# Performance work log

Hardware: AMD Instinct MI355X
Metric: run time of the kernel (lower is better)

## Reference

```python
import jax, jax.numpy as jnp
import numpy as np

LEAK_RATE = 0.1
SPIKE_THRESHOLD = 0.5
MAX_DIM = 2560
R = 2048   # reservoir dim
D = 1024   # input dim
B = 4096   # batch


def setup_inputs() -> dict:
    key = jax.random.key(0)
    k1, k2, k3, k4, k5 = jax.random.split(key, 5)
    inputs = jax.random.normal(k1, (B, D), dtype=jnp.float32)
    prev_state = jax.random.normal(k2, (B, MAX_DIM), dtype=jnp.float32)
    W_in = jax.random.normal(k3, (R, D), dtype=jnp.float32) * (1.0 / np.sqrt(D))
    W_res = jax.random.normal(k4, (R, R), dtype=jnp.float32) * (1.0 / np.sqrt(R))
    W_gate = jax.random.normal(k5, (3 * R, D), dtype=jnp.float32) * (1.0 / np.sqrt(D))
    return {"inputs": inputs, "prev_state": prev_state,
            "W_in": W_in, "W_res": W_res, "W_gate": W_gate}


def reference(inputs, prev_state, W_in, W_res, W_gate):
    # Slice state to active reservoir width (W_res.shape[0] == R)
    prev = prev_state[:, :R]                                  # [B, R]
    input_part = jnp.matmul(inputs, W_in.T)                   # [B, R]
    reservoir_part = jnp.matmul(prev, W_res.T)                # [B, R]
    gate = jax.nn.sigmoid(jnp.matmul(inputs, W_gate.T))       # [B, 3R]
    i_gate, f_gate, o_gate = jnp.split(gate, 3, axis=-1)      # each [B, R]
    state = (1.0 - LEAK_RATE) * (f_gate * prev) \
        + LEAK_RATE * jnp.tanh(i_gate * (input_part + reservoir_part))
    state = o_gate * state
    # Spike threshold + soft reset
    state = jnp.where(state > SPIKE_THRESHOLD, state - SPIKE_THRESHOLD, state)
    # Pad up to max dynamic reservoir dim
    padded = jnp.pad(state, ((0, 0), (0, MAX_DIM - R)))       # [B, MAX_DIM]
    return padded
```

## Files before the change

### kernel.cpp

```cpp
#include <hip/hip_runtime.h>
#include <stdint.h>

#define B_  4096
#define D_  1024
#define R_  2048
#define MAXD 2560

typedef _Float16 half8 __attribute__((ext_vector_type(8)));
typedef _Float16 half4 __attribute__((ext_vector_type(4)));
typedef float    f32x4 __attribute__((ext_vector_type(4)));

constexpr int BM = 128;
constexpr int BN = 64;
constexpr int BK = 32;
constexpr int NCH1 = D_ / BK;
constexpr int NCH2 = R_ / BK;

constexpr size_t XF_OFF  = 0;
constexpr size_t PF_OFF  = XF_OFF  + (size_t)256 * 32 * 2 * 512;
constexpr size_t WIF_OFF = PF_OFF  + (size_t)256 * 64 * 2 * 512;
constexpr size_t WRF_OFF = WIF_OFF + (size_t)128 * 32 * 2 * 512;
constexpr size_t WGF_OFF = WRF_OFF + (size_t)128 * 64 * 2 * 512;
constexpr size_t WS_HALVES = WGF_OFF + (size_t)384 * 32 * 2 * 512;
constexpr size_t WS_BYTES  = WS_HALVES * 2;
constexpr int NPACK_WTASKS = 49152;
constexpr int NPAD_WTASKS  = 8192;

__device__ __forceinline__ float sigmoidf_(float x) { return 1.0f / (1.0f + expf(-x)); }

__device__ __forceinline__ void gload_lds16(const _Float16* g, _Float16* l) {
    typedef const uint32_t __attribute__((address_space(1)))* gp_t;
    typedef uint32_t __attribute__((address_space(3)))* lp_t;
    __builtin_amdgcn_global_load_lds((gp_t)(const void*)g, (lp_t)(void*)l, 16, 0, 0);
}

__global__ __launch_bounds__(256)
void prep(const float* __restrict__ X, const float* __restrict__ P,
          const float* __restrict__ Win, const float* __restrict__ Wres,
          const float* __restrict__ Wg, _Float16* __restrict__ ws,
          float* __restrict__ out)
{
    const int l = threadIdx.x & 63;
    const int wtask = blockIdx.x * 4 + (threadIdx.x >> 6);
    if (wtask < NPACK_WTASKS) {
        const float* src; int ld, rg, kb;
        int cp = wtask;
        if (cp < 8192)       {              src = X;    ld = D_;   rg = cp >> 5; kb = cp & 31; }
        else if (cp < 24576) { cp -= 8192;  src = P;    ld = MAXD; rg = cp >> 6; kb = cp & 63; }
        else if (cp < 28672) { cp -= 24576; src = Win;  ld = D_;   rg = cp >> 5; kb = cp & 31; }
        else if (cp < 36864) { cp -= 28672; src = Wres; ld = R_;   rg = cp >> 6; kb = cp & 63; }
        else                 { cp -= 36864; src = Wg;   ld = D_;   rg = cp >> 5; kb = cp & 31; }
        const float* s = src + (size_t)(rg * 16 + (l & 15)) * ld + kb * 32 + (l >> 4) * 8;
        f32x4 v0 = *(const f32x4*)s;
        f32x4 v1 = *(const f32x4*)(s + 4);
        half8 h, lo;
        #pragma unroll
        for (int j = 0; j < 4; ++j) {
            h[j]     = (_Float16)v0[j];  lo[j]     = (_Float16)(v0[j] - (float)h[j]);
            h[4 + j] = (_Float16)v1[j];  lo[4 + j] = (_Float16)(v1[j] - (float)h[4 + j]);
        }
        _Float16* dst = ws + (size_t)wtask * 1024;
        *(half8*)(dst + l * 8) = h;
        *(half8*)(dst + 512 + l * 8) = lo;
    } else {
        int p2 = wtask - NPACK_WTASKS;
        size_t idx = (size_t)p2 * 256 + l * 4;
        size_t row = idx >> 9, col = idx & 511;
        *(f32x4*)(out + row * MAXD + R_ + col) = (f32x4){0.f, 0.f, 0.f, 0.f};
    }
}

__global__ __launch_bounds__(256, 2)
void reservoir_packed(const _Float16* __restrict__ ws,
                      const float* __restrict__ P,
                      float* __restrict__ out)
{
    __shared__ _Float16 smem[32768];

    const int tid  = threadIdx.x;
    const int lane = tid & 63;
    const int wv   = tid >> 6;
    const int m0   = blockIdx.y * BM;
    const int n0   = blockIdx.x * BN;
    const int lb   = lane * 8;
    const int rgA  = (m0 >> 4) + wv * 2;
    const int ng0  = n0 >> 4;

    f32x4 acc[4][2][4];
    #pragma unroll
    for (int s = 0; s < 4; ++s)
        #pragma unroll
        for (int mt = 0; mt < 2; ++mt)
            #pragma unroll
            for (int nt = 0; nt < 4; ++nt) acc[s][mt][nt] = (f32x4){0.f, 0.f, 0.f, 0.f};

    auto dmaW1 = [&](int t, int buf) {
        #pragma unroll
        for (int i = 0; i < 8; ++i) {
            const int c = wv * 8 + i, pl = c >> 4, r = c & 15, s = r >> 2, g = r & 3;
            const size_t gh = (s == 0)
                ? WIF_OFF + ((size_t)((ng0 + g) * 32 + t) * 2 + pl) * 512
                : WGF_OFF + ((size_t)(((s - 1) * 128 + ng0 + g) * 32 + t) * 2 + pl) * 512;
            gload_lds16(ws + gh + lb, &smem[buf * 16384 + pl * 8192 + r * 512]);
        }
    };
    auto dmaW2 = [&](int t, int buf) {
        #pragma unroll
        for (int i = 0; i < 2; ++i) {
            const int c = wv * 2 + i, pl = c >> 2, g = c & 3;
            const size_t gh = WRF_OFF + ((size_t)((ng0 + g) * 64 + t) * 2 + pl) * 512;
            gload_lds16(ws + gh + lb, &smem[buf * 16384 + pl * 8192 + g * 512]);
        }
    };

#define LDA(ROFF, KBS, T, H0, L0, H1, L1)                                                         \
    {                                                                                             \
        const _Float16* b0_ = ws + (ROFF) + ((size_t)((rgA + 0) * (KBS) + (T)) * 2) * 512 + lb;   \
        const _Float16* b1_ = ws + (ROFF) + ((size_t)((rgA + 1) * (KBS) + (T)) * 2) * 512 + lb;   \
        H0 = *(const half8*)b0_;  L0 = *(const half8*)(b0_ + 512);                                \
        H1 = *(const half8*)b1_;  L1 = *(const half8*)(b1_ + 512);                                \
    }

#define MBLK(BB, NSETS, AH0, AL0, AH1, AL1)                                                       \
    {                                                                                             \
        __builtin_amdgcn_s_setprio(1);                                                            \
        _Pragma("unroll")                                                                         \
        for (int s = 0; s < (NSETS); ++s) {                                                       \
            _Pragma("unroll")                                                                     \
            for (int nt = 0; nt < 4; ++nt) {                                                      \
                half8 bh = *(const half8*)&smem[(BB) + (s * 4 + nt) * 512 + lb];                  \
                half8 bl = *(const half8*)&smem[(BB) + 8192 + (s * 4 + nt) * 512 + lb];           \
                acc[s][0][nt] = __builtin_amdgcn_mfma_f32_16x16x32_f16(AH0, bh, acc[s][0][nt], 0, 0, 0); \
                acc[s][0][nt] = __builtin_amdgcn_mfma_f32_16x16x32_f16(AL0, bh, acc[s][0][nt], 0, 0, 0); \
                acc[s][0][nt] = __builtin_amdgcn_mfma_f32_16x16x32_f16(AH0, bl, acc[s][0][nt], 0, 0, 0); \
                acc[s][1][nt] = __builtin_amdgcn_mfma_f32_16x16x32_f16(AH1, bh, acc[s][1][nt], 0, 0, 0); \
                acc[s][1][nt] = __builtin_amdgcn_mfma_f32_16x16x32_f16(AL1, bh, acc[s][1][nt], 0, 0, 0); \
                acc[s][1][nt] = __builtin_amdgcn_mfma_f32_16x16x32_f16(AH1, bl, acc[s][1][nt], 0, 0, 0); \
            }                                                                                     \
        }                                                                                         \
        __builtin_amdgcn_s_setprio(0);                                                            \
    }

#define BARR()                                                                                    \
    {                                                                                             \
        __builtin_amdgcn_sched_barrier(0);                                                        \
        asm volatile("s_waitcnt vmcnt(4) lgkmcnt(0)" ::: "memory");                               \
        __builtin_amdgcn_s_barrier();                                                             \
        __builtin_amdgcn_sched_barrier(0);                                                        \
    }
#define FENCE() __builtin_amdgcn_sched_barrier(0)

    half8 ah0A, al0A, ah1A, al1A, ah0B, al0B, ah1B, al1B;

    dmaW1(0, 0);
    FENCE();
    LDA(XF_OFF, 32, 0, ah0A, al0A, ah1A, al1A);
    BARR();

    #pragma unroll 1
    for (int t = 0; t < NCH1 - 2; t += 2) {
        dmaW1(t + 1, 1); FENCE(); LDA(XF_OFF, 32, t + 1, ah0B, al0B, ah1B, al1B);
        MBLK(0, 4, ah0A, al0A, ah1A, al1A)
        BARR();
        dmaW1(t + 2, 0); FENCE(); LDA(XF_OFF, 32, t + 2, ah0A, al0A, ah1A, al1A);
        MBLK(16384, 4, ah0B, al0B, ah1B, al1B)
        BARR();
    }
    dmaW1(31, 1); FENCE(); LDA(XF_OFF, 32, 31, ah0B, al0B, ah1B, al1B);
    MBLK(0, 4, ah0A, al0A, ah1A, al1A)
    BARR();
    dmaW2(0, 0); FENCE(); LDA(PF_OFF, 64, 0, ah0A, al0A, ah1A, al1A);
    MBLK(16384, 4, ah0B, al0B, ah1B, al1B)
    BARR();

    #pragma unroll 1
    for (int t = 0; t < NCH2 - 2; t += 2) {
        dmaW2(t + 1, 1); FENCE(); LDA(PF_OFF, 64, t + 1, ah0B, al0B, ah1B, al1B);
        MBLK(0, 1, ah0A, al0A, ah1A, al1A)
        BARR();
        dmaW2(t + 2, 0); FENCE(); LDA(PF_OFF, 64, t + 2, ah0A, al0A, ah1A, al1A);
        MBLK(16384, 1, ah0B, al0B, ah1B, al1B)
        BARR();
    }
    dmaW2(63, 1); FENCE(); LDA(PF_OFF, 64, 63, ah0B, al0B, ah1B, al1B);
    MBLK(0, 1, ah0A, al0A, ah1A, al1A)
    BARR();
    MBLK(16384, 1, ah0B, al0B, ah1B, al1B)

#undef MBLK
#undef LDA
#undef BARR
#undef FENCE

    const int fr = lane & 15;
    const int qd = lane >> 4;
    #pragma unroll
    for (int mt = 0; mt < 2; ++mt)
        #pragma unroll
        for (int nt = 0; nt < 4; ++nt)
            #pragma unroll
            for (int r = 0; r < 4; ++r) {
                int row = m0 + wv * 32 + mt * 16 + qd * 4 + r;
                int col = n0 + nt * 16 + fr;
                float pre = acc[0][mt][nt][r];
                float ig  = sigmoidf_(acc[1][mt][nt][r]);
                float fg  = sigmoidf_(acc[2][mt][nt][r]);
                float og  = sigmoidf_(acc[3][mt][nt][r]);
                float pv  = P[(size_t)row * MAXD + col];
                float st  = 0.9f * (fg * pv) + 0.1f * tanhf(ig * pre);
                st *= og;
                if (st > 0.5f) st -= 0.5f;
                out[(size_t)row * MAXD + col] = st;
            }
}

__device__ __forceinline__ void wg_barrier_ref() {
    __builtin_amdgcn_sched_barrier(0);
    asm volatile("s_waitcnt lgkmcnt(0)" ::: "memory");
    __builtin_amdgcn_s_barrier();
    __builtin_amdgcn_sched_barrier(0);
}

__global__ __launch_bounds__(256, 2)
void reservoir_ref(const float* __restrict__ X, const float* __restrict__ P,
                   const float* __restrict__ Win, const float* __restrict__ Wres,
                   const float* __restrict__ Wg, float* __restrict__ out)
{
    __shared__ _Float16 sA[2][8][512];
    __shared__ _Float16 sW[2][4][4][512];
    const int tid  = threadIdx.x;
    const int lane = tid & 63;
    const int wv   = tid >> 6;
    const int m0   = blockIdx.y * BM;
    const int n0   = blockIdx.x * BN;
    f32x4 acc[4][2][4];
    #pragma unroll
    for (int s = 0; s < 4; ++s)
        #pragma unroll
        for (int mt = 0; mt < 2; ++mt)
            #pragma unroll
            for (int nt = 0; nt < 4; ++nt) acc[s][mt][nt] = (f32x4){0.f, 0.f, 0.f, 0.f};
    const int crow = tid >> 3;
    const int c4   = (tid & 7) * 4;
    const int q    = c4 >> 3;
    const int fbase = q * 128 + (c4 & 4);
    const int raddr = ((((lane & 15) ^ (lane >> 4)) << 3) + ((lane >> 4) << 7));
    f32x4 pa[4];
    f32x4 pw[8];
    auto issue_loads = [&](int t) {
        if (t < NCH1) {
            const int kc = t * BK + c4;
            const float* a = X + (size_t)m0 * D_ + kc;
            #pragma unroll
            for (int i = 0; i < 4; ++i) pa[i] = *(const f32x4*)(a + (size_t)(crow + 32 * i) * D_);
            const float* w = Win + (size_t)n0 * D_ + kc;
            #pragma unroll
            for (int i = 0; i < 2; ++i) pw[i] = *(const f32x4*)(w + (size_t)(crow + 32 * i) * D_);
            const float* g = Wg + (size_t)n0 * D_ + kc;
            #pragma unroll
            for (int gg = 0; gg < 3; ++gg)
                #pragma unroll
                for (int i = 0; i < 2; ++i)
                    pw[2 + gg * 2 + i] = *(const f32x4*)(g + (size_t)(gg * R_ + crow + 32 * i) * D_);
        } else {
            const int kc = t * BK - D_ + c4;
            const float* a = P + (size_t)m0 * MAXD + kc;
            #pragma unroll
            for (int i = 0; i < 4; ++i) pa[i] = *(const f32x4*)(a + (size_t)(crow + 32 * i) * MAXD);
            const float* w = Wres + (size_t)n0 * R_ + kc;
            #pragma unroll
            for (int i = 0; i < 2; ++i) pw[i] = *(const f32x4*)(w + (size_t)(crow + 32 * i) * R_);
        }
    };
    auto stage_A = [&]() {
        #pragma unroll
        for (int i = 0; i < 4; ++i) {
            const int r = crow + 32 * i;
            const int idx = (((r & 15) ^ q) << 3) + fbase;
            half4 h, l;
            #pragma unroll
            for (int j = 0; j < 4; ++j) {
                float v = pa[i][j];
                h[j] = (_Float16)v;
                l[j] = (_Float16)(v - (float)h[j]);
            }
            *(half4*)(&sA[0][r >> 4][idx]) = h;
            *(half4*)(&sA[1][r >> 4][idx]) = l;
        }
    };
    auto stage_W = [&](int nw) {
        #pragma unroll
        for (int i = 0; i < 8; ++i) if (i < nw) {
            const int s   = (i < 2) ? 0 : 1 + ((i - 2) >> 1);
            const int sub = (i < 2) ? i : ((i - 2) & 1);
            const int r   = crow + 32 * sub;
            const int idx = (((r & 15) ^ q) << 3) + fbase;
            half4 h, l;
            #pragma unroll
            for (int j = 0; j < 4; ++j) {
                float v = pw[i][j];
                h[j] = (_Float16)v;
                l[j] = (_Float16)(v - (float)h[j]);
            }
            *(half4*)(&sW[0][s][r >> 4][idx]) = h;
            *(half4*)(&sW[1][s][r >> 4][idx]) = l;
        }
    };
#define RMFMA(NSETS)                                                                              \
    {                                                                                             \
        half8 ah0 = *(const half8*)(&sA[0][wv * 2 + 0][raddr]);                                   \
        half8 al0 = *(const half8*)(&sA[1][wv * 2 + 0][raddr]);                                   \
        half8 ah1 = *(const half8*)(&sA[0][wv * 2 + 1][raddr]);                                   \
        half8 al1 = *(const half8*)(&sA[1][wv * 2 + 1][raddr]);                                   \
        _Pragma("unroll")                                                                         \
        for (int s = 0; s < NSETS; ++s) {                                                         \
            _Pragma("unroll")                                                                     \
            for (int nt = 0; nt < 4; ++nt) {                                                      \
                half8 bh = *(const half8*)(&sW[0][s][nt][raddr]);                                 \
                half8 bl = *(const half8*)(&sW[1][s][nt][raddr]);                                 \
                acc[s][0][nt] = __builtin_amdgcn_mfma_f32_16x16x32_f16(ah0, bh, acc[s][0][nt], 0, 0, 0); \
                acc[s][0][nt] = __builtin_amdgcn_mfma_f32_16x16x32_f16(al0, bh, acc[s][0][nt], 0, 0, 0); \
                acc[s][0][nt] = __builtin_amdgcn_mfma_f32_16x16x32_f16(ah0, bl, acc[s][0][nt], 0, 0, 0); \
                acc[s][1][nt] = __builtin_amdgcn_mfma_f32_16x16x32_f16(ah1, bh, acc[s][1][nt], 0, 0, 0); \
                acc[s][1][nt] = __builtin_amdgcn_mfma_f32_16x16x32_f16(al1, bh, acc[s][1][nt], 0, 0, 0); \
                acc[s][1][nt] = __builtin_amdgcn_mfma_f32_16x16x32_f16(ah1, bl, acc[s][1][nt], 0, 0, 0); \
            }                                                                                     \
        }                                                                                         \
    }
    issue_loads(0);
    #pragma unroll 1
    for (int t = 0; t < NCH1; ++t) {
        stage_A(); stage_W(8);
        issue_loads(t + 1);
        wg_barrier_ref();
        RMFMA(4)
        wg_barrier_ref();
    }
    #pragma unroll 1
    for (int t = NCH1; t < NCH1 + NCH2; ++t) {
        stage_A(); stage_W(2);
        if (t + 1 < NCH1 + NCH2) issue_loads(t + 1);
        wg_barrier_ref();
        RMFMA(1)
        wg_barrier_ref();
    }
#undef RMFMA
    const int fr = lane & 15;
    const int qd = lane >> 4;
    #pragma unroll
    for (int mt = 0; mt < 2; ++mt)
        #pragma unroll
        for (int nt = 0; nt < 4; ++nt)
            #pragma unroll
            for (int r = 0; r < 4; ++r) {
                int row = m0 + wv * 32 + mt * 16 + qd * 4 + r;
                int col = n0 + nt * 16 + fr;
                float pre = acc[0][mt][nt][r];
                float ig  = sigmoidf_(acc[1][mt][nt][r]);
                float fg  = sigmoidf_(acc[2][mt][nt][r]);
                float og  = sigmoidf_(acc[3][mt][nt][r]);
                float pv  = P[(size_t)row * MAXD + col];
                float st  = 0.9f * (fg * pv) + 0.1f * tanhf(ig * pre);
                st *= og;
                if (st > 0.5f) st -= 0.5f;
                out[(size_t)row * MAXD + col] = st;
            }
}

__global__ void pad_zero(float* __restrict__ out) {
    int idx = blockIdx.x * 256 + threadIdx.x;
    int row = idx >> 7;
    int c   = (idx & 127) * 4;
    *(f32x4*)(&out[(size_t)row * MAXD + R_ + c]) = (f32x4){0.f, 0.f, 0.f, 0.f};
}

extern "C" void kernel_launch(void* const* d_in, const int* in_sizes, int n_in,
                              void* d_out, int out_size, void* d_ws, size_t ws_size,
                              hipStream_t stream) {
    const float* X    = (const float*)d_in[0];
    const float* P    = (const float*)d_in[1];
    const float* Win  = (const float*)d_in[2];
    const float* Wres = (const float*)d_in[3];
    const float* Wg   = (const float*)d_in[4];
    float* out        = (float*)d_out;

    dim3 grid(R_ / BN, B_ / BM);

    if (d_ws != nullptr && ws_size >= WS_BYTES) {
        _Float16* ws = (_Float16*)d_ws;
        prep<<<(NPACK_WTASKS + NPAD_WTASKS) / 4, 256, 0, stream>>>(X, P, Win, Wres, Wg, ws, out);
        reservoir_packed<<<grid, 256, 0, stream>>>((const _Float16*)ws, P, out);
    } else {
        pad_zero<<<2048, 256, 0, stream>>>(out);
        reservoir_ref<<<grid, 256, 0, stream>>>(X, P, Win, Wres, Wg, out);
    }
}
```

Before: 421.9 us.

## Split activations to fp16 hi/lo inside GEMM instead of prepacking

```diff
diff --git a/kernel.cpp b/kernel.cpp
--- a/kernel.cpp
+++ b/kernel.cpp
@@ -16,15 +16,13 @@
 constexpr int NCH1 = D_ / BK;
 constexpr int NCH2 = R_ / BK;
 
-constexpr size_t XF_OFF  = 0;
-constexpr size_t PF_OFF  = XF_OFF  + (size_t)256 * 32 * 2 * 512;
-constexpr size_t WIF_OFF = PF_OFF  + (size_t)256 * 64 * 2 * 512;
-constexpr size_t WRF_OFF = WIF_OFF + (size_t)128 * 32 * 2 * 512;
-constexpr size_t WGF_OFF = WRF_OFF + (size_t)128 * 64 * 2 * 512;
-constexpr size_t WS_HALVES = WGF_OFF + (size_t)384 * 32 * 2 * 512;
+constexpr size_t WIF_OFF = 0;
+constexpr size_t WRF_OFF = WIF_OFF + (size_t)128 * 32 * 1024;
+constexpr size_t WGF_OFF = WRF_OFF + (size_t)128 * 64 * 1024;
+constexpr size_t WS_HALVES = WGF_OFF + (size_t)384 * 32 * 1024;
 constexpr size_t WS_BYTES  = WS_HALVES * 2;
-constexpr int NPACK_WTASKS = 49152;
-constexpr int NPAD_WTASKS  = 8192;
+constexpr int NW_TASKS    = 4096 + 8192 + 12288;
+constexpr int NPAD_WTASKS = 8192;
 
 __device__ __forceinline__ float sigmoidf_(float x) { return 1.0f / (1.0f + expf(-x)); }
 
@@ -35,21 +33,18 @@
 }
 
 __global__ __launch_bounds__(256)
-void prep(const float* __restrict__ X, const float* __restrict__ P,
-          const float* __restrict__ Win, const float* __restrict__ Wres,
+void prep(const float* __restrict__ Win, const float* __restrict__ Wres,
           const float* __restrict__ Wg, _Float16* __restrict__ ws,
           float* __restrict__ out)
 {
     const int l = threadIdx.x & 63;
     const int wtask = blockIdx.x * 4 + (threadIdx.x >> 6);
-    if (wtask < NPACK_WTASKS) {
+    if (wtask < NW_TASKS) {
         const float* src; int ld, rg, kb;
         int cp = wtask;
-        if (cp < 8192)       {              src = X;    ld = D_;   rg = cp >> 5; kb = cp & 31; }
-        else if (cp < 24576) { cp -= 8192;  src = P;    ld = MAXD; rg = cp >> 6; kb = cp & 63; }
-        else if (cp < 28672) { cp -= 24576; src = Win;  ld = D_;   rg = cp >> 5; kb = cp & 31; }
-        else if (cp < 36864) { cp -= 28672; src = Wres; ld = R_;   rg = cp >> 6; kb = cp & 63; }
-        else                 { cp -= 36864; src = Wg;   ld = D_;   rg = cp >> 5; kb = cp & 31; }
+        if (cp < 4096)       {              src = Win;  ld = D_; rg = cp >> 5; kb = cp & 31; }
+        else if (cp < 12288) { cp -= 4096;  src = Wres; ld = R_; rg = cp >> 6; kb = cp & 63; }
+        else                 { cp -= 12288; src = Wg;   ld = D_; rg = cp >> 5; kb = cp & 31; }
         const float* s = src + (size_t)(rg * 16 + (l & 15)) * ld + kb * 32 + (l >> 4) * 8;
         f32x4 v0 = *(const f32x4*)s;
         f32x4 v1 = *(const f32x4*)(s + 4);
@@ -63,7 +58,7 @@
         *(half8*)(dst + l * 8) = h;
         *(half8*)(dst + 512 + l * 8) = lo;
     } else {
-        int p2 = wtask - NPACK_WTASKS;
+        int p2 = wtask - NW_TASKS;
         size_t idx = (size_t)p2 * 256 + l * 4;
         size_t row = idx >> 9, col = idx & 511;
         *(f32x4*)(out + row * MAXD + R_ + col) = (f32x4){0.f, 0.f, 0.f, 0.f};
@@ -71,8 +66,9 @@
 }
 
 __global__ __launch_bounds__(256, 2)
-void reservoir_packed(const _Float16* __restrict__ ws,
+void reservoir_packed(const float* __restrict__ X,
                       const float* __restrict__ P,
+                      const _Float16* __restrict__ ws,
                       float* __restrict__ out)
 {
     __shared__ _Float16 smem[32768];
@@ -113,16 +109,26 @@
         }
     };
 
-#define LDA(ROFF, KBS, T, H0, L0, H1, L1)                                                         \
+    const float* aX = X + (size_t)(rgA * 16 + (lane & 15)) * D_   + (lane >> 4) * 8;
+    const float* aP = P + (size_t)(rgA * 16 + (lane & 15)) * MAXD + (lane >> 4) * 8;
+
+#define LDA_RAW(BASE, LD16, T, V0, V1, V2, V3)                                                    \
     {                                                                                             \
-        const _Float16* b0_ = ws + (ROFF) + ((size_t)((rgA + 0) * (KBS) + (T)) * 2) * 512 + lb;   \
-        const _Float16* b1_ = ws + (ROFF) + ((size_t)((rgA + 1) * (KBS) + (T)) * 2) * 512 + lb;   \
-        H0 = *(const half8*)b0_;  L0 = *(const half8*)(b0_ + 512);                                \
-        H1 = *(const half8*)b1_;  L1 = *(const half8*)(b1_ + 512);                                \
-    }
-
-#define MBLK(BB, NSETS, AH0, AL0, AH1, AL1)                                                       \
+        const float* p_ = (BASE) + (size_t)(T) * BK;                                              \
+        V0 = *(const f32x4*)p_;             V1 = *(const f32x4*)(p_ + 4);                         \
+        V2 = *(const f32x4*)(p_ + (LD16));  V3 = *(const f32x4*)(p_ + (LD16) + 4);                \
+    }
+
+#define MBLK(BB, NSETS, V0, V1, V2, V3)                                                           \
     {                                                                                             \
+        half8 ah0, al0, ah1, al1;                                                                 \
+        _Pragma("unroll")                                                                         \
+        for (int j = 0; j < 4; ++j) {                                                             \
+            ah0[j]     = (_Float16)V0[j];  al0[j]     = (_Float16)(V0[j] - (float)ah0[j]);        \
+            ah0[4 + j] = (_Float16)V1[j];  al0[4 + j] = (_Float16)(V1[j] - (float)ah0[4 + j]);    \
+            ah1[j]     = (_Float16)V2[j];  al1[j]     = (_Float16)(V2[j] - (float)ah1[j]);        \
+            ah1[4 + j] = (_Float16)V3[j];  al1[4 + j] = (_Float16)(V3[j] - (float)ah1[4 + j]);    \
+        }                                                                                         \
         __builtin_amdgcn_s_setprio(1);                                                            \
         _Pragma("unroll")                                                                         \
         for (int s = 0; s < (NSETS); ++s) {                                                       \
@@ -130,12 +136,12 @@
             for (int nt = 0; nt < 4; ++nt) {                                                      \
                 half8 bh = *(const half8*)&smem[(BB) + (s * 4 + nt) * 512 + lb];                  \
                 half8 bl = *(const half8*)&smem[(BB) + 8192 + (s * 4 + nt) * 512 + lb];           \
-                acc[s][0][nt] = __builtin_amdgcn_mfma_f32_16x16x32_f16(AH0, bh, acc[s][0][nt], 0, 0, 0); \
-                acc[s][0][nt] = __builtin_amdgcn_mfma_f32_16x16x32_f16(AL0, bh, acc[s][0][nt], 0, 0, 0); \
-                acc[s][0][nt] = __builtin_amdgcn_mfma_f32_16x16x32_f16(AH0, bl, acc[s][0][nt], 0, 0, 0); \
-                acc[s][1][nt] = __builtin_amdgcn_mfma_f32_16x16x32_f16(AH1, bh, acc[s][1][nt], 0, 0, 0); \
-                acc[s][1][nt] = __builtin_amdgcn_mfma_f32_16x16x32_f16(AL1, bh, acc[s][1][nt], 0, 0, 0); \
-                acc[s][1][nt] = __builtin_amdgcn_mfma_f32_16x16x32_f16(AH1, bl, acc[s][1][nt], 0, 0, 0); \
+                acc[s][0][nt] = __builtin_amdgcn_mfma_f32_16x16x32_f16(ah0, bh, acc[s][0][nt], 0, 0, 0); \
+                acc[s][0][nt] = __builtin_amdgcn_mfma_f32_16x16x32_f16(al0, bh, acc[s][0][nt], 0, 0, 0); \
+                acc[s][0][nt] = __builtin_amdgcn_mfma_f32_16x16x32_f16(ah0, bl, acc[s][0][nt], 0, 0, 0); \
+                acc[s][1][nt] = __builtin_amdgcn_mfma_f32_16x16x32_f16(ah1, bh, acc[s][1][nt], 0, 0, 0); \
+                acc[s][1][nt] = __builtin_amdgcn_mfma_f32_16x16x32_f16(al1, bh, acc[s][1][nt], 0, 0, 0); \
+                acc[s][1][nt] = __builtin_amdgcn_mfma_f32_16x16x32_f16(ah1, bl, acc[s][1][nt], 0, 0, 0); \
             }                                                                                     \
         }                                                                                         \
         __builtin_amdgcn_s_setprio(0);                                                            \
@@ -150,45 +156,45 @@
     }
 #define FENCE() __builtin_amdgcn_sched_barrier(0)
 
-    half8 ah0A, al0A, ah1A, al1A, ah0B, al0B, ah1B, al1B;
+    f32x4 xa0, xa1, xa2, xa3, xb0, xb1, xb2, xb3;
 
     dmaW1(0, 0);
     FENCE();
-    LDA(XF_OFF, 32, 0, ah0A, al0A, ah1A, al1A);
+    LDA_RAW(aX, 16 * D_, 0, xa0, xa1, xa2, xa3);
     BARR();
 
     #pragma unroll 1
     for (int t = 0; t < NCH1 - 2; t += 2) {
-        dmaW1(t + 1, 1); FENCE(); LDA(XF_OFF, 32, t + 1, ah0B, al0B, ah1B, al1B);
-        MBLK(0, 4, ah0A, al0A, ah1A, al1A)
+        dmaW1(t + 1, 1); FENCE(); LDA_RAW(aX, 16 * D_, t + 1, xb0, xb1, xb2, xb3);
+        MBLK(0, 4, xa0, xa1, xa2, xa3)
         BARR();
-        dmaW1(t + 2, 0); FENCE(); LDA(XF_OFF, 32, t + 2, ah0A, al0A, ah1A, al1A);
-        MBLK(16384, 4, ah0B, al0B, ah1B, al1B)
+        dmaW1(t + 2, 0); FENCE(); LDA_RAW(aX, 16 * D_, t + 2, xa0, xa1, xa2, xa3);
+        MBLK(16384, 4, xb0, xb1, xb2, xb3)
         BARR();
     }
-    dmaW1(31, 1); FENCE(); LDA(XF_OFF, 32, 31, ah0B, al0B, ah1B, al1B);
-    MBLK(0, 4, ah0A, al0A, ah1A, al1A)
+    dmaW1(31, 1); FENCE(); LDA_RAW(aX, 16 * D_, 31, xb0, xb1, xb2, xb3);
+    MBLK(0, 4, xa0, xa1, xa2, xa3)
     BARR();
-    dmaW2(0, 0); FENCE(); LDA(PF_OFF, 64, 0, ah0A, al0A, ah1A, al1A);
-    MBLK(16384, 4, ah0B, al0B, ah1B, al1B)
+    dmaW2(0, 0); FENCE(); LDA_RAW(aP, 16 * MAXD, 0, xa0, xa1, xa2, xa3);
+    MBLK(16384, 4, xb0, xb1, xb2, xb3)
     BARR();
 
     #pragma unroll 1
     for (int t = 0; t < NCH2 - 2; t += 2) {
-        dmaW2(t + 1, 1); FENCE(); LDA(PF_OFF, 64, t + 1, ah0B, al0B, ah1B, al1B);
-        MBLK(0, 1, ah0A, al0A, ah1A, al1A)
+        dmaW2(t + 1, 1); FENCE(); LDA_RAW(aP, 16 * MAXD, t + 1, xb0, xb1, xb2, xb3);
+        MBLK(0, 1, xa0, xa1, xa2, xa3)
         BARR();
-        dmaW2(t + 2, 0); FENCE(); LDA(PF_OFF, 64, t + 2, ah0A, al0A, ah1A, al1A);
-        MBLK(16384, 1, ah0B, al0B, ah1B, al1B)
+        dmaW2(t + 2, 0); FENCE(); LDA_RAW(aP, 16 * MAXD, t + 2, xa0, xa1, xa2, xa3);
+        MBLK(16384, 1, xb0, xb1, xb2, xb3)
         BARR();
     }
-    dmaW2(63, 1); FENCE(); LDA(PF_OFF, 64, 63, ah0B, al0B, ah1B, al1B);
-    MBLK(0, 1, ah0A, al0A, ah1A, al1A)
+    dmaW2(63, 1); FENCE(); LDA_RAW(aP, 16 * MAXD, 63, xb0, xb1, xb2, xb3);
+    MBLK(0, 1, xa0, xa1, xa2, xa3)
     BARR();
-    MBLK(16384, 1, ah0B, al0B, ah1B, al1B)
+    MBLK(16384, 1, xb0, xb1, xb2, xb3)
 
 #undef MBLK
-#undef LDA
+#undef LDA_RAW
 #undef BARR
 #undef FENCE
 
@@ -388,8 +394,8 @@
 
     if (d_ws != nullptr && ws_size >= WS_BYTES) {
         _Float16* ws = (_Float16*)d_ws;
-        prep<<<(NPACK_WTASKS + NPAD_WTASKS) / 4, 256, 0, stream>>>(X, P, Win, Wres, Wg, ws, out);
-        reservoir_packed<<<grid, 256, 0, stream>>>((const _Float16*)ws, P, out);
+        prep<<<(NW_TASKS + NPAD_WTASKS) / 4, 256, 0, stream>>>(Win, Wres, Wg, ws, out);
+        reservoir_packed<<<grid, 256, 0, stream>>>(X, P, (const _Float16*)ws, out);
     } else {
         pad_zero<<<2048, 256, 0, stream>>>(out);
         reservoir_ref<<<grid, 256, 0, stream>>>(X, P, Win, Wres, Wg, out);
```

After: 465.4 us. 1.1x slower.
